# Kernel optimization log

Measured on AMD Instinct MI355X. Metric: run time of the kernel, lower is better.

The kernel has to match this reference:

```python
import jax, jax.numpy as jnp
import numpy as np

B, J, HID, NG = 16384, 16, 128, 5
NEG = -9e15
EDGES = [(0,1),(1,2),(2,3),(0,4),(4,5),(5,6),(0,7),(7,8),(8,9),(9,10),(8,11),(11,12),(12,13),(8,14),(14,15)]

def _skeleton_mask():
    m = np.eye(J, dtype=bool)
    for i, j in EDGES:
        m[i, j] = True
        m[j, i] = True
    return jnp.asarray(m)

def setup_inputs() -> dict:
    key = jax.random.key(0)
    ks = jax.random.split(key, 8)
    s = 0.05
    ones, zeros = jnp.ones(HID), jnp.zeros(HID)
    bn = jnp.stack([ones, zeros, zeros, ones])  # gamma, beta, running_mean, running_var
    return {
        "x": jax.random.normal(ks[0], (B, J, 2), jnp.float32),
        "W_in": jax.random.normal(ks[1], (2, 2, HID), jnp.float32) * s,
        "e_in": jax.random.normal(ks[2], (J, J), jnp.float32),
        "b_in": jnp.zeros((HID,), jnp.float32),
        "bn_in": bn,
        "W_mid": jax.random.normal(ks[3], (8, 2, HID, HID), jnp.float32) * s,
        "e_mid": jax.random.normal(ks[4], (8, J, J), jnp.float32),
        "b_mid": jnp.zeros((8, HID), jnp.float32),
        "bn_mid": jnp.broadcast_to(bn, (8, 4, HID)),
        "W_out": jax.random.normal(ks[5], (2, HID, NG * 5), jnp.float32) * s,
        "e_out": jax.random.normal(ks[6], (J, J), jnp.float32),
        "b_out": jnp.zeros((NG * 5,), jnp.float32),
        "adj_mask": _skeleton_mask(),
    }

def _semgconv(x, W, e, b, mask):
    # x: [B,J,Cin]; W: [2,Cin,Cout]; e: [J,J] attention logits on adjacency support
    h0 = jnp.einsum('bjc,cf->bjf', x, W[0])  # self transform
    h1 = jnp.einsum('bjc,cf->bjf', x, W[1])  # neighbor transform
    A = jax.nn.softmax(jnp.where(mask, e, NEG), axis=1)  # [J,J]
    eye = jnp.eye(mask.shape[0], dtype=A.dtype)
    out = jnp.einsum('ij,bjf->bif', A * eye, h0) + jnp.einsum('ij,bjf->bif', A * (1.0 - eye), h1)
    return out + b

def _bn_relu(h, bn):
    gamma, beta, mean, var = bn[0], bn[1], bn[2], bn[3]
    return jax.nn.relu((h - mean) * jax.lax.rsqrt(var + 1e-5) * gamma + beta)

def reference(x, W_in, e_in, b_in, bn_in, W_mid, e_mid, b_mid, bn_mid, W_out, e_out, b_out, adj_mask):
    h = _bn_relu(_semgconv(x, W_in, e_in, b_in, adj_mask), bn_in)
    for i in range(4):  # 4 residual blocks, each with 2 gconvs
        r = h
        for k in (2 * i, 2 * i + 1):
            h = _bn_relu(_semgconv(h, W_mid[k], e_mid[k], b_mid[k], adj_mask), bn_mid[k])
        h = r + h
    out = _semgconv(h, W_out, e_out, b_out, adj_mask)  # [B,J,25]
    mu = jnp.tanh(out[:, :, : NG * 3].reshape(out.shape[0], out.shape[1], NG, 3))
    sigma = out[:, :, NG * 3 : NG * 4][:, :, :, None]
    pi = out[:, :, NG * 4 : NG * 5]
    sigma = jnp.maximum(jax.nn.elu(sigma) + 1.0, 1e-10)
    return mu, sigma, pi
```

## Files before the change

kernel.cpp:

```cpp
#include <hip/hip_runtime.h>


typedef unsigned short u16;
typedef short s16x8 __attribute__((ext_vector_type(8)));
typedef unsigned short u16x4 __attribute__((ext_vector_type(4)));
typedef float f32x4 __attribute__((ext_vector_type(4)));
typedef float f32x2 __attribute__((ext_vector_type(2)));
typedef _Float16 f16x4 __attribute__((ext_vector_type(4)));

#define BATCH 16384
#define BT 8

#define MU_OFF (BATCH * 16 * 15)
#define SG_OFF (BATCH * 16 * 5)

#define WS_WTO 524288
#define WS_A   540672
#define WS_S   550912
#define WS_T   555520
#define WS_BP  560128

__device__ __forceinline__ float b2f(u16 b) {
  unsigned u = ((unsigned)b) << 16; float f; __builtin_memcpy(&f, &u, 4); return f;
}
__device__ __forceinline__ u16 f2b(float f) {
  unsigned u; __builtin_memcpy(&u, &f, 4);
  u = (u + 0x7fffu + ((u >> 16) & 1u)) >> 16;
  return (u16)u;
}
__device__ __forceinline__ bool dtyf32(const void* bnin) {
  return *(const unsigned*)bnin == 0x3F800000u;
}
__device__ __forceinline__ float ldf(const void* p, int i, bool f32) {
  return f32 ? ((const float*)p)[i] : b2f(((const u16*)p)[i]);
}
__device__ __forceinline__ _Float16 tof16(float v) {
  return (_Float16)fminf(fmaxf(v, -60000.f), 60000.f);
}
__device__ __forceinline__ f32x4 mm32(s16x8 a, s16x8 b, f32x4 c) {
  return __builtin_amdgcn_mfma_f32_16x16x32_bf16(a, b, c, 0, 0, 0);
}
__device__ __forceinline__ f32x4 mm16(f16x4 a, f16x4 b, f32x4 c) {
  return __builtin_amdgcn_mfma_f32_16x16x16f16(a, b, c, 0, 0, 0);
}

__device__ const u16 MASKBITS[16] = {
  0x0093, 0x0007, 0x000E, 0x000C, 0x0031, 0x0070, 0x0060, 0x0181,
  0x4B80, 0x0700, 0x0600, 0x1900, 0x3800, 0x3000, 0xC100, 0xC000
};

__global__ void prep_kernel(const void* __restrict__ Wmid, const void* __restrict__ Wout,
                            const void* __restrict__ ein,  const void* __restrict__ emid,
                            const void* __restrict__ eout, const void* __restrict__ bnin,
                            const void* __restrict__ bnmid, const void* __restrict__ bin,
                            const void* __restrict__ bmid, const void* __restrict__ bout,
                            u16* __restrict__ WT, u16* __restrict__ WTo,
                            float* __restrict__ A, float* __restrict__ S,
                            float* __restrict__ T, float* __restrict__ bpad) {
  const bool F32 = dtyf32(bnin);
  int tid = blockIdx.x * 256 + threadIdx.x;
  if (tid < 262144) {
    int kk = tid & 127, f = (tid >> 7) & 127, lm = tid >> 14;
    WT[((lm << 7) + f) * 128 + kk] = f2b(ldf(Wmid, ((lm << 7) + kk) * 128 + f, F32));
  } else if (tid < 262144 + 8192) {
    int t2 = tid - 262144;
    int kk = t2 & 127, f = (t2 >> 7) & 31, m = t2 >> 12;
    WTo[((m * 32 + f) << 7) + kk] =
        (f < 25) ? f2b(ldf(Wout, (m * 128 + kk) * 25 + f, F32)) : (u16)0;
  } else if (tid < 262144 + 8192 + 160) {
    int t3 = tid - (262144 + 8192);
    int i = t3 & 15, L = t3 >> 4;
    const void* e = (L == 0) ? ein : (L <= 8 ? emid : eout);
    int ebase = (L >= 1 && L <= 8) ? (L - 1) * 256 : 0;
    unsigned mrow = MASKBITS[i];
    float v[16]; float mx = -1e30f;
    for (int j = 0; j < 16; j++) {
      v[j] = ldf(e, ebase + i * 16 + j, F32);
      if ((mrow >> j) & 1) mx = fmaxf(mx, v[j]);
    }
    float sum = 0.f;
    for (int j = 0; j < 16; j++) {
      if ((mrow >> j) & 1) { v[j] = expf(v[j] - mx); sum += v[j]; } else v[j] = 0.f;
    }
    float inv = 1.f / sum;
    for (int j = 0; j < 16; j++) A[L * 256 + i * 16 + j] = v[j] * inv;
  } else if (tid < 262144 + 8192 + 160 + 1152) {
    int t4 = tid - (262144 + 8192 + 160);
    int f = t4 & 127, L = t4 >> 7;
    float gam, bet, mea, var, bb;
    if (L == 0) {
      gam = ldf(bnin, f, F32);       bet = ldf(bnin, 128 + f, F32);
      mea = ldf(bnin, 256 + f, F32); var = ldf(bnin, 384 + f, F32);
      bb  = ldf(bin, f, F32);
    } else {
      int k = L - 1; int bo_ = k * 512;
      gam = ldf(bnmid, bo_ + f, F32);       bet = ldf(bnmid, bo_ + 128 + f, F32);
      mea = ldf(bnmid, bo_ + 256 + f, F32); var = ldf(bnmid, bo_ + 384 + f, F32);
      bb  = ldf(bmid, k * 128 + f, F32);
    }
    float s = gam * rsqrtf(var + 1e-5f);
    S[L * 128 + f] = s;
    T[L * 128 + f] = (bb - mea) * s + bet;
  } else if (tid < 262144 + 8192 + 160 + 1152 + 32) {
    int f = tid - (262144 + 8192 + 160 + 1152);
    bpad[f] = (f < 25) ? ldf(bout, f, F32) : 0.f;
  }
}

__global__ __launch_bounds__(512, 4) void semgcn_main(
    const void* __restrict__ x, const void* __restrict__ Win,
    const u16* __restrict__ WT, const u16* __restrict__ WTo,
    const float* __restrict__ A, const float* __restrict__ S,
    const float* __restrict__ T, const float* __restrict__ bpad,
    const void* __restrict__ bnin, void* __restrict__ out) {
  __shared__ __align__(16) u16 hbuf[2 * 128 * 128];
  const bool F32 = dtyf32(bnin);
  const int tid = threadIdx.x;
  const int w = tid >> 6, lane = tid & 63, q = lane >> 4, n = lane & 15;
  const int bbase = blockIdx.x * BT;
  const int Fb = 16 * w;
  const int rswz = n & 7;
  const f32x4 zf = {0.f, 0.f, 0.f, 0.f};

  {
    float w00, w01, w10, w11;
    {
      int f = Fb + n;
      w00 = ldf(Win, f, F32);        w01 = ldf(Win, 128 + f, F32);
      w10 = ldf(Win, 256 + f, F32);  w11 = ldf(Win, 384 + f, F32);
    }
    f16x4 bd, bo;
    {
      const f32x4 ar = *(const f32x4*)(A + n * 16 + 4 * q);
#pragma unroll
      for (int r = 0; r < 4; r++) {
        int j = 4 * q + r;
        bd[r] = (j == n) ? (_Float16)ar[r] : (_Float16)0.f;
        bo[r] = (j != n) ? (_Float16)ar[r] : (_Float16)0.f;
      }
    }
    f32x4 Sv = *(const f32x4*)(S + Fb + 4 * q);
    f32x4 Tv = *(const f32x4*)(T + Fb + 4 * q);
    for (int c = 0; c < BT; c++) {
      int b = bbase + c;
      float x0[4], x1[4];
#pragma unroll
      for (int r = 0; r < 4; r++) {
        int j = b * 16 + 4 * q + r;
        if (F32) {
          f32x2 xv = *(const f32x2*)((const float*)x + j * 2);
          x0[r] = xv[0]; x1[r] = xv[1];
        } else {
          unsigned xv = *(const unsigned*)((const u16*)x + j * 2);
          x0[r] = b2f((u16)(xv & 0xffffu));
          x1[r] = b2f((u16)(xv >> 16));
        }
      }
      int R = c * 16 + n;
      f16x4 a0, a1;
#pragma unroll
      for (int r = 0; r < 4; r++) {
        a0[r] = tof16(x0[r] * w00 + x1[r] * w01);
        a1[r] = tof16(x0[r] * w10 + x1[r] * w11);
      }
      f32x4 o = mm16(a0, bd, zf);
      o = mm16(a1, bo, o);
      int f = Fb + 4 * q;
      int off = R * 128 + (((f >> 3) ^ rswz) << 3) + (f & 7);
      u16x4 st;
#pragma unroll
      for (int r = 0; r < 4; r++) {
        float v = fmaxf(o[r] * Sv[r] + Tv[r], 0.f);
        st[r] = f2b(v);
      }
      *(u16x4*)&hbuf[off] = st;
    }
  }
  __syncthreads();

  for (int kl = 0; kl < 8; kl++) {
    const int bufR = (kl & 1) * 16384;
    const int bufW = ((kl + 1) & 1) * 16384;
    s16x8 wf[2][4];
#pragma unroll
    for (int m = 0; m < 2; m++)
#pragma unroll
      for (int s = 0; s < 4; s++)
        wf[m][s] = *(const s16x8*)(WT + ((((kl * 2 + m) << 7) + Fb + n) << 7)
                                   + 32 * s + 8 * q);
    f16x4 bd, bo;
    {
      const f32x4 ar = *(const f32x4*)(A + (kl + 1) * 256 + n * 16 + 4 * q);
#pragma unroll
      for (int r = 0; r < 4; r++) {
        int j = 4 * q + r;
        bd[r] = (j == n) ? (_Float16)ar[r] : (_Float16)0.f;
        bo[r] = (j != n) ? (_Float16)ar[r] : (_Float16)0.f;
      }
    }
    f32x4 Sv = *(const f32x4*)(S + (kl + 1) * 128 + Fb + 4 * q);
    f32x4 Tv = *(const f32x4*)(T + (kl + 1) * 128 + Fb + 4 * q);
    for (int c = 0; c < BT; c++) {
      int R = c * 16 + n;
      s16x8 hf[4];
#pragma unroll
      for (int s = 0; s < 4; s++) {
        int off = R * 128 + (((4 * s + q) ^ rswz) << 3);
        hf[s] = *(const s16x8*)&hbuf[bufR + off];
      }
      f32x4 acc0 = zf, acc1 = zf;
#pragma unroll
      for (int s = 0; s < 4; s++) {
        acc0 = mm32(hf[s], wf[0][s], acc0);
        acc1 = mm32(hf[s], wf[1][s], acc1);
      }
      f16x4 a0, a1;
#pragma unroll
      for (int r = 0; r < 4; r++) {
        a0[r] = tof16(acc0[r]);
        a1[r] = tof16(acc1[r]);
      }
      f32x4 o = mm16(a0, bd, zf);
      o = mm16(a1, bo, o);
      int f = Fb + 4 * q;
      int off = R * 128 + (((f >> 3) ^ rswz) << 3) + (f & 7);
      float v0 = fmaxf(o[0] * Sv[0] + Tv[0], 0.f);
      float v1 = fmaxf(o[1] * Sv[1] + Tv[1], 0.f);
      float v2 = fmaxf(o[2] * Sv[2] + Tv[2], 0.f);
      float v3 = fmaxf(o[3] * Sv[3] + Tv[3], 0.f);
      if (kl & 1) {
        u16x4 rr = *(const u16x4*)&hbuf[bufW + off];
        v0 += b2f(rr[0]); v1 += b2f(rr[1]); v2 += b2f(rr[2]); v3 += b2f(rr[3]);
      }
      u16x4 st = { f2b(v0), f2b(v1), f2b(v2), f2b(v3) };
      *(u16x4*)&hbuf[bufW + off] = st;
    }
    __syncthreads();
  }

  {
    int c = w;
    int b = bbase + c;
    int R = c * 16 + n;
    s16x8 hf[4];
#pragma unroll
    for (int s = 0; s < 4; s++) {
      int off = R * 128 + (((4 * s + q) ^ rswz) << 3);
      hf[s] = *(const s16x8*)&hbuf[off];
    }
    f16x4 bd, bo;
    {
      const f32x4 ar = *(const f32x4*)(A + 9 * 256 + n * 16 + 4 * q);
#pragma unroll
      for (int r = 0; r < 4; r++) {
        int j = 4 * q + r;
        bd[r] = (j == n) ? (_Float16)ar[r] : (_Float16)0.f;
        bo[r] = (j != n) ? (_Float16)ar[r] : (_Float16)0.f;
      }
    }
#pragma unroll
    for (int t = 0; t < 2; t++) {
      s16x8 wo0[4], wo1[4];
#pragma unroll
      for (int s = 0; s < 4; s++) {
        wo0[s] = *(const s16x8*)(WTo + ((0 * 32 + 16 * t + n) << 7) + 32 * s + 8 * q);
        wo1[s] = *(const s16x8*)(WTo + ((1 * 32 + 16 * t + n) << 7) + 32 * s + 8 * q);
      }
      f32x4 acc0 = zf, acc1 = zf;
#pragma unroll
      for (int s = 0; s < 4; s++) {
        acc0 = mm32(hf[s], wo0[s], acc0);
        acc1 = mm32(hf[s], wo1[s], acc1);
      }
      f16x4 a0, a1;
#pragma unroll
      for (int r = 0; r < 4; r++) {
        a0[r] = tof16(acc0[r]);
        a1[r] = tof16(acc1[r]);
      }
      f32x4 o = mm16(a0, bd, zf);
      o = mm16(a1, bo, o);
      f32x4 bv = *(const f32x4*)(bpad + 16 * t + 4 * q);
      int row = b * 16 + n;
#pragma unroll
      for (int r = 0; r < 4; r++) {
        int f = 16 * t + 4 * q + r;
        float v = o[r] + bv[r];
        int idx = -1; float val = 0.f;
        if (f < 15) {
          idx = row * 15 + f;                    val = tanhf(v);
        } else if (f < 20) {
          float sg = (v > 0.f) ? (v + 1.f) : expf(v);
          idx = MU_OFF + row * 5 + (f - 15);     val = fmaxf(sg, 1e-10f);
        } else if (f < 25) {
          idx = MU_OFF + SG_OFF + row * 5 + (f - 20); val = v;
        }
        if (idx >= 0) {
          if (F32) ((float*)out)[idx] = val;
          else     ((u16*)out)[idx]   = f2b(val);
        }
      }
    }
  }
}

extern "C" void kernel_launch(void* const* d_in, const int* in_sizes, int n_in,
                              void* d_out, int out_size, void* d_ws, size_t ws_size,
                              hipStream_t stream) {
  const void* x     = d_in[0];
  const void* Win   = d_in[1];
  const void* ein   = d_in[2];
  const void* bin   = d_in[3];
  const void* bnin  = d_in[4];
  const void* Wmid  = d_in[5];
  const void* emid  = d_in[6];
  const void* bmid  = d_in[7];
  const void* bnmid = d_in[8];
  const void* Wout  = d_in[9];
  const void* eout  = d_in[10];
  const void* bout  = d_in[11];

  char* ws = (char*)d_ws;
  u16*   WT   = (u16*)(ws);
  u16*   WTo  = (u16*)(ws + WS_WTO);
  float* A    = (float*)(ws + WS_A);
  float* S    = (float*)(ws + WS_S);
  float* T    = (float*)(ws + WS_T);
  float* bpad = (float*)(ws + WS_BP);

  prep_kernel<<<1062, 256, 0, stream>>>(Wmid, Wout, ein, emid, eout, bnin, bnmid,
                                        bin, bmid, bout, WT, WTo, A, S, T, bpad);
  semgcn_main<<<BATCH / BT, 512, 0, stream>>>(x, Win, WT, WTo, A, S, T, bpad,
                                              bnin, (u16*)d_out);
}
```

Baseline: 331.8 us.

## Switch activations to fp16, halve batch tile, and split output heads across waves

Stores hidden activations and weights as fp16 instead of bf16 and uses the f16 MFMA for the feature GEMMs. This drops the clamp-based fp16 conversions between the two MFMA stages. The batch tile shrinks from 8 to 4 samples per block, halving LDS use, and launch bounds rise to 8 blocks per SM to raise occupancy. The final layer now spreads its two 16-column output halves across 8 waves instead of looping, at the cost of fp16 overflow risk without the clamps and twice as many blocks, each reloading the weights.

Measured after the change: 586.7 us. +76.8%, slower.

```diff
diff --git a/kernel.cpp b/kernel.cpp
--- a/kernel.cpp
+++ b/kernel.cpp
@@ -2,14 +2,14 @@
 
 
 typedef unsigned short u16;
-typedef short s16x8 __attribute__((ext_vector_type(8)));
 typedef unsigned short u16x4 __attribute__((ext_vector_type(4)));
 typedef float f32x4 __attribute__((ext_vector_type(4)));
 typedef float f32x2 __attribute__((ext_vector_type(2)));
 typedef _Float16 f16x4 __attribute__((ext_vector_type(4)));
+typedef _Float16 f16x8 __attribute__((ext_vector_type(8)));
 
 #define BATCH 16384
-#define BT 8
+#define BT 4
 
 #define MU_OFF (BATCH * 16 * 15)
 #define SG_OFF (BATCH * 16 * 5)
@@ -28,17 +28,20 @@
   u = (u + 0x7fffu + ((u >> 16) & 1u)) >> 16;
   return (u16)u;
 }
+__device__ __forceinline__ u16 f2h(float f) {
+  _Float16 h = (_Float16)f; u16 b; __builtin_memcpy(&b, &h, 2); return b;
+}
+__device__ __forceinline__ float h2f(u16 b) {
+  _Float16 h; __builtin_memcpy(&h, &b, 2); return (float)h;
+}
 __device__ __forceinline__ bool dtyf32(const void* bnin) {
   return *(const unsigned*)bnin == 0x3F800000u;
 }
 __device__ __forceinline__ float ldf(const void* p, int i, bool f32) {
   return f32 ? ((const float*)p)[i] : b2f(((const u16*)p)[i]);
 }
-__device__ __forceinline__ _Float16 tof16(float v) {
-  return (_Float16)fminf(fmaxf(v, -60000.f), 60000.f);
-}
-__device__ __forceinline__ f32x4 mm32(s16x8 a, s16x8 b, f32x4 c) {
-  return __builtin_amdgcn_mfma_f32_16x16x32_bf16(a, b, c, 0, 0, 0);
+__device__ __forceinline__ f32x4 mm32(f16x8 a, f16x8 b, f32x4 c) {
+  return __builtin_amdgcn_mfma_f32_16x16x32_f16(a, b, c, 0, 0, 0);
 }
 __device__ __forceinline__ f32x4 mm16(f16x4 a, f16x4 b, f32x4 c) {
   return __builtin_amdgcn_mfma_f32_16x16x16f16(a, b, c, 0, 0, 0);
@@ -61,12 +64,12 @@
   int tid = blockIdx.x * 256 + threadIdx.x;
   if (tid < 262144) {
     int kk = tid & 127, f = (tid >> 7) & 127, lm = tid >> 14;
-    WT[((lm << 7) + f) * 128 + kk] = f2b(ldf(Wmid, ((lm << 7) + kk) * 128 + f, F32));
+    WT[((lm << 7) + f) * 128 + kk] = f2h(ldf(Wmid, ((lm << 7) + kk) * 128 + f, F32));
   } else if (tid < 262144 + 8192) {
     int t2 = tid - 262144;
     int kk = t2 & 127, f = (t2 >> 7) & 31, m = t2 >> 12;
     WTo[((m * 32 + f) << 7) + kk] =
-        (f < 25) ? f2b(ldf(Wout, (m * 128 + kk) * 25 + f, F32)) : (u16)0;
+        (f < 25) ? f2h(ldf(Wout, (m * 128 + kk) * 25 + f, F32)) : (u16)0;
   } else if (tid < 262144 + 8192 + 160) {
     int t3 = tid - (262144 + 8192);
     int i = t3 & 15, L = t3 >> 4;
@@ -107,13 +110,13 @@
   }
 }
 
-__global__ __launch_bounds__(512, 4) void semgcn_main(
+__global__ __launch_bounds__(512, 8) void semgcn_main(
     const void* __restrict__ x, const void* __restrict__ Win,
     const u16* __restrict__ WT, const u16* __restrict__ WTo,
     const float* __restrict__ A, const float* __restrict__ S,
     const float* __restrict__ T, const float* __restrict__ bpad,
     const void* __restrict__ bnin, void* __restrict__ out) {
-  __shared__ __align__(16) u16 hbuf[2 * 128 * 128];
+  __shared__ __align__(16) u16 hbuf[2 * 64 * 128];
   const bool F32 = dtyf32(bnin);
   const int tid = threadIdx.x;
   const int w = tid >> 6, lane = tid & 63, q = lane >> 4, n = lane & 15;
@@ -160,8 +163,8 @@
       f16x4 a0, a1;
 #pragma unroll
       for (int r = 0; r < 4; r++) {
-        a0[r] = tof16(x0[r] * w00 + x1[r] * w01);
-        a1[r] = tof16(x0[r] * w10 + x1[r] * w11);
+        a0[r] = (_Float16)(x0[r] * w00 + x1[r] * w01);
+        a1[r] = (_Float16)(x0[r] * w10 + x1[r] * w11);
       }
       f32x4 o = mm16(a0, bd, zf);
       o = mm16(a1, bo, o);
@@ -171,7 +174,7 @@
 #pragma unroll
       for (int r = 0; r < 4; r++) {
         float v = fmaxf(o[r] * Sv[r] + Tv[r], 0.f);
-        st[r] = f2b(v);
+        st[r] = f2h(v);
       }
       *(u16x4*)&hbuf[off] = st;
     }
@@ -179,14 +182,14 @@
   __syncthreads();
 
   for (int kl = 0; kl < 8; kl++) {
-    const int bufR = (kl & 1) * 16384;
-    const int bufW = ((kl + 1) & 1) * 16384;
-    s16x8 wf[2][4];
+    const int bufR = (kl & 1) * 8192;
+    const int bufW = ((kl + 1) & 1) * 8192;
+    f16x8 wf[2][4];
 #pragma unroll
     for (int m = 0; m < 2; m++)
 #pragma unroll
       for (int s = 0; s < 4; s++)
-        wf[m][s] = *(const s16x8*)(WT + ((((kl * 2 + m) << 7) + Fb + n) << 7)
+        wf[m][s] = *(const f16x8*)(WT + ((((kl * 2 + m) << 7) + Fb + n) << 7)
                                    + 32 * s + 8 * q);
     f16x4 bd, bo;
     {
@@ -202,11 +205,11 @@
     f32x4 Tv = *(const f32x4*)(T + (kl + 1) * 128 + Fb + 4 * q);
     for (int c = 0; c < BT; c++) {
       int R = c * 16 + n;
-      s16x8 hf[4];
+      f16x8 hf[4];
 #pragma unroll
       for (int s = 0; s < 4; s++) {
         int off = R * 128 + (((4 * s + q) ^ rswz) << 3);
-        hf[s] = *(const s16x8*)&hbuf[bufR + off];
+        hf[s] = *(const f16x8*)&hbuf[bufR + off];
       }
       f32x4 acc0 = zf, acc1 = zf;
 #pragma unroll
@@ -217,8 +220,8 @@
       f16x4 a0, a1;
 #pragma unroll
       for (int r = 0; r < 4; r++) {
-        a0[r] = tof16(acc0[r]);
-        a1[r] = tof16(acc1[r]);
+        a0[r] = (_Float16)acc0[r];
+        a1[r] = (_Float16)acc1[r];
       }
       f32x4 o = mm16(a0, bd, zf);
       o = mm16(a1, bo, o);
@@ -230,23 +233,24 @@
       float v3 = fmaxf(o[3] * Sv[3] + Tv[3], 0.f);
       if (kl & 1) {
         u16x4 rr = *(const u16x4*)&hbuf[bufW + off];
-        v0 += b2f(rr[0]); v1 += b2f(rr[1]); v2 += b2f(rr[2]); v3 += b2f(rr[3]);
-      }
-      u16x4 st = { f2b(v0), f2b(v1), f2b(v2), f2b(v3) };
+        v0 += h2f(rr[0]); v1 += h2f(rr[1]); v2 += h2f(rr[2]); v3 += h2f(rr[3]);
+      }
+      u16x4 st = { f2h(v0), f2h(v1), f2h(v2), f2h(v3) };
       *(u16x4*)&hbuf[bufW + off] = st;
     }
     __syncthreads();
   }
 
   {
-    int c = w;
+    int c = w & 3;
+    int t = w >> 2;
     int b = bbase + c;
     int R = c * 16 + n;
-    s16x8 hf[4];
+    f16x8 hf[4];
 #pragma unroll
     for (int s = 0; s < 4; s++) {
       int off = R * 128 + (((4 * s + q) ^ rswz) << 3);
-      hf[s] = *(const s16x8*)&hbuf[off];
+      hf[s] = *(const f16x8*)&hbuf[off];
     }
     f16x4 bd, bo;
     {
@@ -258,47 +262,44 @@
         bo[r] = (j != n) ? (_Float16)ar[r] : (_Float16)0.f;
       }
     }
-#pragma unroll
-    for (int t = 0; t < 2; t++) {
-      s16x8 wo0[4], wo1[4];
-#pragma unroll
-      for (int s = 0; s < 4; s++) {
-        wo0[s] = *(const s16x8*)(WTo + ((0 * 32 + 16 * t + n) << 7) + 32 * s + 8 * q);
-        wo1[s] = *(const s16x8*)(WTo + ((1 * 32 + 16 * t + n) << 7) + 32 * s + 8 * q);
-      }
-      f32x4 acc0 = zf, acc1 = zf;
-#pragma unroll
-      for (int s = 0; s < 4; s++) {
-        acc0 = mm32(hf[s], wo0[s], acc0);
-        acc1 = mm32(hf[s], wo1[s], acc1);
-      }
-      f16x4 a0, a1;
-#pragma unroll
-      for (int r = 0; r < 4; r++) {
-        a0[r] = tof16(acc0[r]);
-        a1[r] = tof16(acc1[r]);
-      }
-      f32x4 o = mm16(a0, bd, zf);
-      o = mm16(a1, bo, o);
-      f32x4 bv = *(const f32x4*)(bpad + 16 * t + 4 * q);
-      int row = b * 16 + n;
-#pragma unroll
-      for (int r = 0; r < 4; r++) {
-        int f = 16 * t + 4 * q + r;
-        float v = o[r] + bv[r];
-        int idx = -1; float val = 0.f;
-        if (f < 15) {
-          idx = row * 15 + f;                    val = tanhf(v);
-        } else if (f < 20) {
-          float sg = (v > 0.f) ? (v + 1.f) : expf(v);
-          idx = MU_OFF + row * 5 + (f - 15);     val = fmaxf(sg, 1e-10f);
-        } else if (f < 25) {
-          idx = MU_OFF + SG_OFF + row * 5 + (f - 20); val = v;
-        }
-        if (idx >= 0) {
-          if (F32) ((float*)out)[idx] = val;
-          else     ((u16*)out)[idx]   = f2b(val);
-        }
+    f16x8 wo0[4], wo1[4];
+#pragma unroll
+    for (int s = 0; s < 4; s++) {
+      wo0[s] = *(const f16x8*)(WTo + ((0 * 32 + 16 * t + n) << 7) + 32 * s + 8 * q);
+      wo1[s] = *(const f16x8*)(WTo + ((1 * 32 + 16 * t + n) << 7) + 32 * s + 8 * q);
+    }
+    f32x4 acc0 = zf, acc1 = zf;
+#pragma unroll
+    for (int s = 0; s < 4; s++) {
+      acc0 = mm32(hf[s], wo0[s], acc0);
+      acc1 = mm32(hf[s], wo1[s], acc1);
+    }
+    f16x4 a0, a1;
+#pragma unroll
+    for (int r = 0; r < 4; r++) {
+      a0[r] = (_Float16)acc0[r];
+      a1[r] = (_Float16)acc1[r];
+    }
+    f32x4 o = mm16(a0, bd, zf);
+    o = mm16(a1, bo, o);
+    f32x4 bv = *(const f32x4*)(bpad + 16 * t + 4 * q);
+    int row = b * 16 + n;
+#pragma unroll
+    for (int r = 0; r < 4; r++) {
+      int f = 16 * t + 4 * q + r;
+      float v = o[r] + bv[r];
+      int idx = -1; float val = 0.f;
+      if (f < 15) {
+        idx = row * 15 + f;                    val = tanhf(v);
+      } else if (f < 20) {
+        float sg = (v > 0.f) ? (v + 1.f) : expf(v);
+        idx = MU_OFF + row * 5 + (f - 15);     val = fmaxf(sg, 1e-10f);
+      } else if (f < 25) {
+        idx = MU_OFF + SG_OFF + row * 5 + (f - 20); val = v;
+      }
+      if (idx >= 0) {
+        if (F32) ((float*)out)[idx] = val;
+        else     ((u16*)out)[idx]   = f2b(val);
       }
     }
   }
```
